# Performance work log

Measured on AMD Instinct MI355X. Metric: run time of the kernel, lower is better.

The kernel has to match this reference:

```python
import jax, jax.numpy as jnp
import numpy as np

N_HEADS = 16  # must match init_kwargs
BIAS_SCALE = 0.1


def _src_grid(out_size, in_size):
    # torch F.interpolate bilinear, align_corners=False semantics
    scale = in_size / out_size
    src = jnp.clip((jnp.arange(out_size, dtype=jnp.float32) + 0.5) * scale - 0.5, 0.0)
    i0 = jnp.minimum(jnp.floor(src).astype(jnp.int32), in_size - 1)
    i1 = jnp.minimum(i0 + 1, in_size - 1)
    w = src - i0.astype(jnp.float32)
    return i0, i1, w


def _bilinear_resize(img, out_h, out_w):
    Hin, Win = img.shape[-2], img.shape[-1]
    r0, r1, wy = _src_grid(out_h, Hin)
    c0, c1, wx = _src_grid(out_w, Win)
    rows = img[:, r0, :] * (1.0 - wy)[None, :, None] + img[:, r1, :] * wy[None, :, None]
    return rows[:, :, c0] * (1.0 - wx)[None, None, :] + rows[:, :, c1] * wx[None, None, :]


def setup_inputs() -> dict:
    key = jax.random.key(0)
    ks = jax.random.split(key, 10)
    B, L, D, M, K = 4, 1024, 1024, 64, 32
    s = 0.02
    return {
        "x": jax.random.normal(ks[0], (B, L, D), dtype=jnp.float32),
        "harmonics": jax.random.normal(ks[1], (B, M, K), dtype=jnp.float32),
        "wq": jax.random.normal(ks[2], (D, D), dtype=jnp.float32) * s,
        "bq": jax.random.normal(ks[3], (D,), dtype=jnp.float32) * s,
        "wk": jax.random.normal(ks[4], (D, D), dtype=jnp.float32) * s,
        "bk": jax.random.normal(ks[5], (D,), dtype=jnp.float32) * s,
        "wv": jax.random.normal(ks[6], (D, D), dtype=jnp.float32) * s,
        "bv": jax.random.normal(ks[7], (D,), dtype=jnp.float32) * s,
        "wo": jax.random.normal(ks[8], (D, D), dtype=jnp.float32) * s,
        "bo": jax.random.normal(ks[9], (D,), dtype=jnp.float32) * s,
    }


def reference(x, harmonics, wq, bq, wk, bk, wv, bv, wo, bo):
    B, L, D = x.shape
    hd = D // N_HEADS
    scaling = hd ** -0.5

    def split_heads(t):  # [B, L, D] -> [B, H, L, hd]
        return t.reshape(B, L, N_HEADS, hd).transpose(0, 2, 1, 3)

    q = split_heads(x @ wq.T + bq)
    k = split_heads(x @ wk.T + bk)
    v = split_heads(x @ wv.T + bv)

    scores = jnp.einsum("bhqd,bhkd->bhqk", q, k) * scaling  # [B, H, L, L]

    gram = jnp.einsum("bmk,bnk->bmn", harmonics, harmonics)  # [B, M, M]
    bias = _bilinear_resize(gram, L, L)  # [B, L, L]
    scores = scores + BIAS_SCALE * bias[:, None, :, :]

    attn = jax.nn.softmax(scores, axis=-1)
    out = jnp.einsum("bhqk,bhkd->bhqd", attn, v)  # [B, H, L, hd]
    out = out.transpose(0, 2, 1, 3).reshape(B, L, D)
    return out @ wo.T + bo
```

## Files before the change

### kernel.cpp

```cpp
#include <hip/hip_runtime.h>


using short8  = __attribute__((ext_vector_type(8))) short;
using short4v = __attribute__((ext_vector_type(4))) short;
using float4v = __attribute__((ext_vector_type(4))) float;

#define MFMA16(a, b, c) __builtin_amdgcn_mfma_f32_16x16x32_bf16((a), (b), (c), 0, 0, 0)

#define LOG2E 1.44269504088896f

static __device__ __forceinline__ short f2bf(float f) {
    union { float f; unsigned u; } v; v.f = f;
    unsigned r = v.u + 0x7fffu + ((v.u >> 16) & 1u);
    return (short)(r >> 16);
}

static __device__ __forceinline__ unsigned pack2bf(float lo, float hi) {
    union { float f; unsigned u; } a, b;
    a.f = lo; b.f = hi;
    return __builtin_amdgcn_perm(b.u + 0x8000u, a.u + 0x8000u, 0x07060302u);
}

static __device__ __forceinline__ void dma16(const short* g, short* l) {
    __builtin_amdgcn_global_load_lds((const __attribute__((address_space(1))) void*)g,
                                     (__attribute__((address_space(3))) void*)l, 16, 0, 0);
}

__global__ __launch_bounds__(256) void convert_all(
    const float* __restrict__ x,  const float* __restrict__ wq,
    const float* __restrict__ wk, const float* __restrict__ wv,
    const float* __restrict__ wo, short* __restrict__ xb, short* __restrict__ wb) {
    int idx = blockIdx.x * 256 + threadIdx.x;
    for (int i = idx; i < 2097152; i += gridDim.x * 256) {
        const float* src; short* dst;
        if (i < 1048576) {
            src = x + (size_t)i * 4;
            dst = xb + (size_t)i * 4;
        } else {
            int j = i - 1048576;
            int sel = j >> 18;
            const float* w = (sel == 0) ? wq : (sel == 1) ? wk : (sel == 2) ? wv : wo;
            src = w + (size_t)(j & 262143) * 4;
            dst = wb + (size_t)j * 4;
        }
        float4v v = *(const float4v*)src;
        short4v o;
        o.x = f2bf(v.x); o.y = f2bf(v.y); o.z = f2bf(v.z); o.w = f2bf(v.w);
        *(short4v*)dst = o;
    }
}

__global__ __launch_bounds__(256) void fill_aug(const float* __restrict__ harm,
                                                short* __restrict__ Qp,
                                                short* __restrict__ Kp) {
    int b  = blockIdx.y;
    int lc = blockIdx.x;
    int tid = threadIdx.x;
    int ll = tid >> 3;
    int d8 = (tid & 7) * 8;
    int l  = lc * 32 + ll;

    __shared__ float hs[64][33];
    for (int i = tid; i < 2048; i += 256) hs[i >> 5][i & 31] = harm[(size_t)b * 2048 + i];
    __syncthreads();

    float src = (l + 0.5f) * 0.0625f - 0.5f;
    if (src < 0.f) src = 0.f;
    int r0 = (int)floorf(src); if (r0 > 63) r0 = 63;
    int r1 = r0 + 1;           if (r1 > 63) r1 = 63;
    float wy = src - (float)r0;

    float hr[32];
    #pragma unroll
    for (int k = 0; k < 32; k++) hr[k] = (1.f - wy) * hs[r0][k] + wy * hs[r1][k];

    short8 qa, ka;
    #pragma unroll
    for (int j = 0; j < 8; j++) {
        float g = 0.f;
        #pragma unroll
        for (int k = 0; k < 32; k++) g += hr[k] * hs[d8 + j][k];
        qa[j] = f2bf(0.1f * LOG2E * g);
    }
    #pragma unroll
    for (int j = 0; j < 8; j++) {
        float vv = 0.f;
        if (d8 + j == r0) vv += 1.f - wy;
        if (d8 + j == r1) vv += wy;
        ka[j] = f2bf(vv);
    }
    for (int h = 0; h < 16; h++) {
        size_t base = (((size_t)(b * 16 + h) * 1024 + l) << 7) + 64 + d8;
        *(short8*)(Qp + base) = qa;
        *(short8*)(Kp + base) = ka;
    }
}

template <int MODE>
__global__ __launch_bounds__(256, 3) void gemm_kernel(
    const short* __restrict__ A,
    const short* __restrict__ Wb,
    const float* __restrict__ B0, const float* __restrict__ B1, const float* __restrict__ B2,
    short* __restrict__ Qp, short* __restrict__ Kp, short* __restrict__ Vp,
    float* __restrict__ outF) {
    const int z = blockIdx.z;
    const short* W  = Wb + (size_t)z * 1048576;
    const float* Bs = (z == 0) ? B0 : ((z == 1) ? B1 : B2);

    __shared__ short Sm[3][8192];

    const int tid  = threadIdx.x;
    const int lane = tid & 63;
    const int wv   = tid >> 6;
    const int wm   = (wv >> 1) * 64;
    const int wn   = (wv & 1) * 64;
    const int l16  = lane & 15;
    const int quad = lane >> 4;
    const int bm   = blockIdx.x * 128;
    const int bn   = blockIdx.y * 128;

    const short* aSrc[2];
    const short* wSrc[2];
    #pragma unroll
    for (int j = 0; j < 2; j++) {
        int c = j * 256 + tid;
        int r = c >> 2, gs = (c & 3) ^ ((r >> 1) & 3);
        aSrc[j] = A + (size_t)(bm + r) * 1024 + gs * 8;
        wSrc[j] = W + (size_t)(bn + r) * 1024 + gs * 8;
    }
    const int fr = (quad ^ ((l16 >> 1) & 3)) * 8;
    int ai[4], bi[4];
    #pragma unroll
    for (int t = 0; t < 4; t++) {
        ai[t] = (wm + t * 16 + l16) * 32 + fr;
        bi[t] = 4096 + (wn + t * 16 + l16) * 32 + fr;
    }

    float4v zero4 = {0.f, 0.f, 0.f, 0.f};
    float4v acc[4][4];
    #pragma unroll
    for (int i = 0; i < 4; i++)
        #pragma unroll
        for (int j = 0; j < 4; j++) acc[i][j] = zero4;

    dma16(aSrc[0], &Sm[0][wv * 512]);
    dma16(aSrc[1], &Sm[0][2048 + wv * 512]);
    dma16(wSrc[0], &Sm[0][4096 + wv * 512]);
    dma16(wSrc[1], &Sm[0][6144 + wv * 512]);
    #pragma unroll
    for (int j = 0; j < 2; j++) { aSrc[j] += 32; wSrc[j] += 32; }
    dma16(aSrc[0], &Sm[1][wv * 512]);
    dma16(aSrc[1], &Sm[1][2048 + wv * 512]);
    dma16(wSrc[0], &Sm[1][4096 + wv * 512]);
    dma16(wSrc[1], &Sm[1][6144 + wv * 512]);
    #pragma unroll
    for (int j = 0; j < 2; j++) { aSrc[j] += 32; wSrc[j] += 32; }

    asm volatile("s_waitcnt vmcnt(4)" ::: "memory");
    __builtin_amdgcn_s_barrier();
    __builtin_amdgcn_sched_barrier(0);

    int bufR = 0;
    int bufW = 2;

    for (int kt = 0; kt < 32; kt++) {
        if (kt < 30) {
            short* wbuf = &Sm[bufW][0];
            dma16(aSrc[0], wbuf + wv * 512);
            dma16(aSrc[1], wbuf + 2048 + wv * 512);
            dma16(wSrc[0], wbuf + 4096 + wv * 512);
            dma16(wSrc[1], wbuf + 6144 + wv * 512);
            #pragma unroll
            for (int j = 0; j < 2; j++) { aSrc[j] += 32; wSrc[j] += 32; }
        }

        const short* rbuf = &Sm[bufR][0];
        short8 af[4], bfr[4];
        #pragma unroll
        for (int mt = 0; mt < 4; mt++) af[mt]  = *(const short8*)&rbuf[ai[mt]];
        #pragma unroll
        for (int nt = 0; nt < 4; nt++) bfr[nt] = *(const short8*)&rbuf[bi[nt]];
        #pragma unroll
        for (int mt = 0; mt < 4; mt++)
            #pragma unroll
            for (int nt = 0; nt < 4; nt++)
                acc[mt][nt] = MFMA16(af[mt], bfr[nt], acc[mt][nt]);

        if (kt < 31) {
            if (kt < 30) {
                asm volatile("s_waitcnt vmcnt(4)" ::: "memory");
            } else {
                asm volatile("s_waitcnt vmcnt(0)" ::: "memory");
            }
            __builtin_amdgcn_s_barrier();
            __builtin_amdgcn_sched_barrier(0);
        }
        bufR = (bufR >= 2) ? 0 : bufR + 1;
        bufW = (bufW >= 2) ? 0 : bufW + 1;
    }

    #pragma unroll
    for (int mt = 0; mt < 4; mt++)
        #pragma unroll
        for (int nt = 0; nt < 4; nt++) {
            int col = bn + wn + nt * 16 + l16;
            float bias = Bs[col];
            #pragma unroll
            for (int r = 0; r < 4; r++) {
                int row = bm + wm + mt * 16 + quad * 4 + r;
                float val = acc[mt][nt][r] + bias;
                if (MODE == 1) {
                    outF[(size_t)row * 1024 + col] = val;
                } else {
                    int b = row >> 10, l = row & 1023;
                    int h = col >> 6,  d = col & 63;
                    size_t bhl = (size_t)(b * 16 + h) * 1024 + l;
                    if (z == 0)      Qp[(bhl << 7) + d] = f2bf(val * (0.125f * LOG2E));
                    else if (z == 1) Kp[(bhl << 7) + d] = f2bf(val);
                    else {
                        int slot = (l & ~31) | (((l >> 2) & 3) << 3) |
                                   (((l >> 4) & 1) << 2) | (l & 3);
                        Vp[(((size_t)(b * 16 + h) * 64 + d) << 10) + slot] = f2bf(val);
                    }
                }
            }
        }
}

__global__ __launch_bounds__(256, 2)
void flash_kernel(const short* __restrict__ Qp,
                  const short* __restrict__ Kp,
                  const short* __restrict__ Vp,
                  short* __restrict__ AO) {
    const int h  = blockIdx.x;
    const int qb = blockIdx.y;
    const int b  = blockIdx.z;
    const int tid  = threadIdx.x;
    const int lane = tid & 63;
    const int w    = tid >> 6;
    const int l16  = lane & 15;
    const int quad = lane >> 4;
    const size_t bh = (size_t)(b * 16 + h);

    __shared__ short Ks[24576];
    __shared__ short Vs[12288];

    short8 qf[2][4];
    #pragma unroll
    for (int u = 0; u < 2; u++) {
        const short* Qb = Qp + ((bh * 1024 + qb * 128 + w * 32 + u * 16 + l16) << 7) + quad * 8;
        #pragma unroll
        for (int c = 0; c < 4; c++) qf[u][c] = *(const short8*)(Qb + c * 32);
    }

    const short* kSrc[4];
    #pragma unroll
    for (int jj = 0; jj < 4; jj++) {
        int key = w * 16 + jj * 4 + quad;
        kSrc[jj] = Kp + (bh << 17) + key * 128 + ((l16 ^ (key & 15)) * 8);
    }
    const short* vSrc[2];
    #pragma unroll
    for (int g = 0; g < 2; g++) {
        int d = w * 16 + g * 8 + (lane >> 3);
        vSrc[g] = Vp + (bh << 16) + d * 1024 + (((lane & 7) ^ (d & 7)) * 8);
    }

    int krd[4];
    #pragma unroll
    for (int c = 0; c < 4; c++) krd[c] = l16 * 128 + (((c * 4 + quad) ^ l16) * 8);
    int vrd[2];
    #pragma unroll
    for (int g = 0; g < 2; g++) vrd[g] = l16 * 64 + (((g * 4 + quad) ^ (l16 & 7)) * 8);

    #pragma unroll
    for (int jj = 0; jj < 4; jj++) dma16(kSrc[jj], &Ks[w * 2048 + jj * 512]);
    #pragma unroll
    for (int g = 0; g < 2; g++) dma16(vSrc[g], &Vs[w * 1024 + g * 512]);
    #pragma unroll
    for (int jj = 0; jj < 4; jj++) kSrc[jj] += 8192;
    #pragma unroll
    for (int g = 0; g < 2; g++) vSrc[g] += 64;
    #pragma unroll
    for (int jj = 0; jj < 4; jj++) dma16(kSrc[jj], &Ks[8192 + w * 2048 + jj * 512]);
    #pragma unroll
    for (int g = 0; g < 2; g++) dma16(vSrc[g], &Vs[4096 + w * 1024 + g * 512]);
    #pragma unroll
    for (int jj = 0; jj < 4; jj++) kSrc[jj] += 8192;
    #pragma unroll
    for (int g = 0; g < 2; g++) vSrc[g] += 64;

    float4v zero4 = {0.f, 0.f, 0.f, 0.f};
    float4v o_acc[2][4];
    #pragma unroll
    for (int u = 0; u < 2; u++)
        #pragma unroll
        for (int mt = 0; mt < 4; mt++) o_acc[u][mt] = zero4;
    float4v l_acc[2] = {zero4, zero4};

    asm volatile("s_waitcnt vmcnt(6)" ::: "memory");
    __builtin_amdgcn_s_barrier();
    __builtin_amdgcn_sched_barrier(0);

    int bufR = 0;
    int bufW = 2;

    for (int kt = 0; kt < 16; kt++) {
        if (kt < 14) {
            const int wb = bufW << 13;
            const int wv2 = bufW << 12;
            #pragma unroll
            for (int jj = 0; jj < 4; jj++) dma16(kSrc[jj], &Ks[wb + w * 2048 + jj * 512]);
            #pragma unroll
            for (int g = 0; g < 2; g++) dma16(vSrc[g], &Vs[wv2 + w * 1024 + g * 512]);
            #pragma unroll
            for (int jj = 0; jj < 4; jj++) kSrc[jj] += 8192;
            #pragma unroll
            for (int g = 0; g < 2; g++) vSrc[g] += 64;
        }
        const int kb = bufR << 13;
        const int vb = bufR << 12;

        float4v s[2][4];
        #pragma unroll
        for (int mt = 0; mt < 4; mt++) {
            short8 kf[4];
            #pragma unroll
            for (int c = 0; c < 4; c++) kf[c] = *(const short8*)&Ks[kb + krd[c] + mt * 2048];
            #pragma unroll
            for (int u = 0; u < 2; u++) {
                s[u][mt] = MFMA16(kf[0], qf[u][0], zero4);
                #pragma unroll
                for (int c = 1; c < 4; c++)
                    s[u][mt] = MFMA16(kf[c], qf[u][c], s[u][mt]);
            }
        }

        #pragma unroll
        for (int u = 0; u < 2; u++)
            #pragma unroll
            for (int mt = 0; mt < 4; mt++) {
                #pragma unroll
                for (int r = 0; r < 4; r++)
                    s[u][mt][r] = __builtin_exp2f(s[u][mt][r]);
                #pragma unroll
                for (int r = 0; r < 4; r++)
                    l_acc[u][r] += s[u][mt][r];
            }

        #pragma unroll
        for (int g = 0; g < 2; g++) {
            short8 pf[2];
            #pragma unroll
            for (int u = 0; u < 2; u++) {
                union { unsigned uu[4]; short8 v; } t;
                t.uu[0] = pack2bf(s[u][2 * g][0], s[u][2 * g][1]);
                t.uu[1] = pack2bf(s[u][2 * g][2], s[u][2 * g][3]);
                t.uu[2] = pack2bf(s[u][2 * g + 1][0], s[u][2 * g + 1][1]);
                t.uu[3] = pack2bf(s[u][2 * g + 1][2], s[u][2 * g + 1][3]);
                pf[u] = t.v;
            }
            #pragma unroll
            for (int mt = 0; mt < 4; mt++) {
                short8 vf = *(const short8*)&Vs[vb + vrd[g] + mt * 1024];
                #pragma unroll
                for (int u = 0; u < 2; u++)
                    o_acc[u][mt] = MFMA16(vf, pf[u], o_acc[u][mt]);
            }
        }

        if (kt < 15) {
            if (kt < 14) {
                asm volatile("s_waitcnt vmcnt(6)" ::: "memory");
            } else {
                asm volatile("s_waitcnt vmcnt(0)" ::: "memory");
            }
            __builtin_amdgcn_s_barrier();
            __builtin_amdgcn_sched_barrier(0);
        }
        bufR = (bufR >= 2) ? 0 : bufR + 1;
        bufW = (bufW >= 2) ? 0 : bufW + 1;
    }

    #pragma unroll
    for (int u = 0; u < 2; u++) {
        float l = l_acc[u][0] + l_acc[u][1] + l_acc[u][2] + l_acc[u][3];
        l += __shfl_xor(l, 16, 64);
        l += __shfl_xor(l, 32, 64);
        float inv = 1.0f / l;
        int row = b * 1024 + qb * 128 + w * 32 + u * 16 + l16;
        #pragma unroll
        for (int mt = 0; mt < 4; mt++) {
            short4v ov;
            #pragma unroll
            for (int r = 0; r < 4; r++) ov[r] = f2bf(o_acc[u][mt][r] * inv);
            *(short4v*)(AO + (size_t)row * 1024 + h * 64 + mt * 16 + quad * 4) = ov;
        }
    }
}

extern "C" void kernel_launch(void* const* d_in, const int* in_sizes, int n_in,
                              void* d_out, int out_size, void* d_ws, size_t ws_size,
                              hipStream_t stream) {
    const float* x    = (const float*)d_in[0];
    const float* harm = (const float*)d_in[1];
    const float* wq   = (const float*)d_in[2];
    const float* bq   = (const float*)d_in[3];
    const float* wk   = (const float*)d_in[4];
    const float* bk   = (const float*)d_in[5];
    const float* wv   = (const float*)d_in[6];
    const float* bv   = (const float*)d_in[7];
    const float* wo   = (const float*)d_in[8];
    const float* bo   = (const float*)d_in[9];
    float* outF = (float*)d_out;

    short* xb   = (short*)d_ws;
    short* Qp   = xb + (size_t)4 * 1048576;
    short* Kp   = Qp + (size_t)8 * 1048576;
    short* Vp   = Kp + (size_t)8 * 1048576;
    short* Wqkv = Vp + (size_t)4 * 1048576;
    short* Wob  = Wqkv + (size_t)3 * 1048576;
    short* AO   = xb;

    convert_all<<<dim3(2048), dim3(256), 0, stream>>>(x, wq, wk, wv, wo, xb, Wqkv);
    gemm_kernel<0><<<dim3(32, 8, 3), dim3(256), 0, stream>>>(
        xb, Wqkv, bq, bk, bv, Qp, Kp, Vp, nullptr);
    fill_aug<<<dim3(32, 4), dim3(256), 0, stream>>>(harm, Qp, Kp);
    flash_kernel<<<dim3(16, 8, 4), dim3(256), 0, stream>>>(Qp, Kp, Vp, AO);
    gemm_kernel<1><<<dim3(32, 8, 1), dim3(256), 0, stream>>>(
        AO, Wob, bo, nullptr, nullptr, nullptr, nullptr, nullptr, outF);
}
```

Before: 192.9 us.

## Load K and V fragments directly from global memory instead of LDS pipeline

Removes the shared-memory triple-buffered DMA pipeline for K and V tiles in the flash attention kernel, along with its barriers and waitcnts. Each wave now reads its K and V MFMA fragments straight from global memory (through cache) every key tile. This removes LDS traffic and block-wide synchronisation and frees LDS. In exchange, each of the four waves fetches the full K/V tiles redundantly, with no explicit prefetch to hide global latency.

```diff
diff --git a/kernel.cpp b/kernel.cpp
--- a/kernel.cpp
+++ b/kernel.cpp
@@ -242,9 +242,6 @@
     const int quad = lane >> 4;
     const size_t bh = (size_t)(b * 16 + h);
 
-    __shared__ short Ks[24576];
-    __shared__ short Vs[12288];
-
     short8 qf[2][4];
     #pragma unroll
     for (int u = 0; u < 2; u++) {
@@ -253,42 +250,8 @@
         for (int c = 0; c < 4; c++) qf[u][c] = *(const short8*)(Qb + c * 32);
     }
 
-    const short* kSrc[4];
-    #pragma unroll
-    for (int jj = 0; jj < 4; jj++) {
-        int key = w * 16 + jj * 4 + quad;
-        kSrc[jj] = Kp + (bh << 17) + key * 128 + ((l16 ^ (key & 15)) * 8);
-    }
-    const short* vSrc[2];
-    #pragma unroll
-    for (int g = 0; g < 2; g++) {
-        int d = w * 16 + g * 8 + (lane >> 3);
-        vSrc[g] = Vp + (bh << 16) + d * 1024 + (((lane & 7) ^ (d & 7)) * 8);
-    }
-
-    int krd[4];
-    #pragma unroll
-    for (int c = 0; c < 4; c++) krd[c] = l16 * 128 + (((c * 4 + quad) ^ l16) * 8);
-    int vrd[2];
-    #pragma unroll
-    for (int g = 0; g < 2; g++) vrd[g] = l16 * 64 + (((g * 4 + quad) ^ (l16 & 7)) * 8);
-
-    #pragma unroll
-    for (int jj = 0; jj < 4; jj++) dma16(kSrc[jj], &Ks[w * 2048 + jj * 512]);
-    #pragma unroll
-    for (int g = 0; g < 2; g++) dma16(vSrc[g], &Vs[w * 1024 + g * 512]);
-    #pragma unroll
-    for (int jj = 0; jj < 4; jj++) kSrc[jj] += 8192;
-    #pragma unroll
-    for (int g = 0; g < 2; g++) vSrc[g] += 64;
-    #pragma unroll
-    for (int jj = 0; jj < 4; jj++) dma16(kSrc[jj], &Ks[8192 + w * 2048 + jj * 512]);
-    #pragma unroll
-    for (int g = 0; g < 2; g++) dma16(vSrc[g], &Vs[4096 + w * 1024 + g * 512]);
-    #pragma unroll
-    for (int jj = 0; jj < 4; jj++) kSrc[jj] += 8192;
-    #pragma unroll
-    for (int g = 0; g < 2; g++) vSrc[g] += 64;
+    const short* kBase = Kp + (bh << 17) + l16 * 128 + quad * 8;
+    const short* vBase = Vp + (bh << 16) + l16 * 1024 + quad * 8;
 
     float4v zero4 = {0.f, 0.f, 0.f, 0.f};
     float4v o_acc[2][4];
@@ -298,43 +261,33 @@
         for (int mt = 0; mt < 4; mt++) o_acc[u][mt] = zero4;
     float4v l_acc[2] = {zero4, zero4};
 
-    asm volatile("s_waitcnt vmcnt(6)" ::: "memory");
-    __builtin_amdgcn_s_barrier();
-    __builtin_amdgcn_sched_barrier(0);
-
-    int bufR = 0;
-    int bufW = 2;
-
     for (int kt = 0; kt < 16; kt++) {
-        if (kt < 14) {
-            const int wb = bufW << 13;
-            const int wv2 = bufW << 12;
-            #pragma unroll
-            for (int jj = 0; jj < 4; jj++) dma16(kSrc[jj], &Ks[wb + w * 2048 + jj * 512]);
-            #pragma unroll
-            for (int g = 0; g < 2; g++) dma16(vSrc[g], &Vs[wv2 + w * 1024 + g * 512]);
-            #pragma unroll
-            for (int jj = 0; jj < 4; jj++) kSrc[jj] += 8192;
-            #pragma unroll
-            for (int g = 0; g < 2; g++) vSrc[g] += 64;
-        }
-        const int kb = bufR << 13;
-        const int vb = bufR << 12;
+        const short* kT = kBase + kt * 8192;
+        short8 kf[4][4];
+        #pragma unroll
+        for (int mt = 0; mt < 4; mt++)
+            #pragma unroll
+            for (int c = 0; c < 4; c++)
+                kf[mt][c] = *(const short8*)(kT + mt * 2048 + c * 32);
 
         float4v s[2][4];
         #pragma unroll
-        for (int mt = 0; mt < 4; mt++) {
-            short8 kf[4];
-            #pragma unroll
-            for (int c = 0; c < 4; c++) kf[c] = *(const short8*)&Ks[kb + krd[c] + mt * 2048];
+        for (int mt = 0; mt < 4; mt++)
             #pragma unroll
             for (int u = 0; u < 2; u++) {
-                s[u][mt] = MFMA16(kf[0], qf[u][0], zero4);
+                s[u][mt] = MFMA16(kf[mt][0], qf[u][0], zero4);
                 #pragma unroll
                 for (int c = 1; c < 4; c++)
-                    s[u][mt] = MFMA16(kf[c], qf[u][c], s[u][mt]);
-            }
-        }
+                    s[u][mt] = MFMA16(kf[mt][c], qf[u][c], s[u][mt]);
+            }
+
+        const short* vT = vBase + kt * 64;
+        short8 vf[2][4];
+        #pragma unroll
+        for (int g = 0; g < 2; g++)
+            #pragma unroll
+            for (int mt = 0; mt < 4; mt++)
+                vf[g][mt] = *(const short8*)(vT + mt * 16384 + g * 32);
 
         #pragma unroll
         for (int u = 0; u < 2; u++)
@@ -361,25 +314,11 @@
                 pf[u] = t.v;
             }
             #pragma unroll
-            for (int mt = 0; mt < 4; mt++) {
-                short8 vf = *(const short8*)&Vs[vb + vrd[g] + mt * 1024];
+            for (int mt = 0; mt < 4; mt++)
                 #pragma unroll
                 for (int u = 0; u < 2; u++)
-                    o_acc[u][mt] = MFMA16(vf, pf[u], o_acc[u][mt]);
-            }
-        }
-
-        if (kt < 15) {
-            if (kt < 14) {
-                asm volatile("s_waitcnt vmcnt(6)" ::: "memory");
-            } else {
-                asm volatile("s_waitcnt vmcnt(0)" ::: "memory");
-            }
-            __builtin_amdgcn_s_barrier();
-            __builtin_amdgcn_sched_barrier(0);
-        }
-        bufR = (bufR >= 2) ? 0 : bufR + 1;
-        bufW = (bufW >= 2) ? 0 : bufW + 1;
+                    o_acc[u][mt] = MFMA16(vf[g][mt], pf[u], o_acc[u][mt]);
+        }
     }
 
     #pragma unroll
```

Measured after the change: 241.1 us. +25.0%, slower.
